# Optimization experiments

Measured on AMD Instinct MI355X. Metric: run time of the kernel, lower is better.

Reference implementation:

```python
import jax, jax.numpy as jnp
import numpy as np

GRID_SIZE = 5
GRID_RANGE = (-1.0, 1.0)


def setup_inputs() -> dict:
    key = jax.random.key(0)
    k1, k2, k3 = jax.random.split(key, 3)
    B, D, U, K = 16384, 1024, 128, GRID_SIZE + 3  # spline_order=3
    x = jax.random.normal(k1, (B, D), dtype=jnp.float32)
    # glorot-ish scale for weights
    base_weight = jax.random.normal(k2, (D, U), dtype=jnp.float32) * (1.0 / np.sqrt(D))
    spline_weight = jax.random.normal(k3, (D, U, K), dtype=jnp.float32) * (1.0 / np.sqrt(D))
    return {"x": x, "base_weight": base_weight, "spline_weight": spline_weight}


def reference(x, base_weight, spline_weight):
    # base path: SiLU(x @ W_b)
    base_out = jax.nn.silu(x @ base_weight)  # [B, U]
    # spline path: RBF over grid centers, then contract (note: x_norm in the
    # original call() is computed but unused, so it is omitted here)
    centers = jnp.linspace(GRID_RANGE[0], GRID_RANGE[1], GRID_SIZE)  # [G]
    dist = jnp.square(x[..., None] - centers)        # [B, D, G]
    rbf = jnp.exp(-5.0 * dist)                        # [B, D, G]
    spline_out = jnp.einsum('big,iug->bu', rbf, spline_weight[:, :, :GRID_SIZE])
    return base_out + spline_out
```

## Files before the change

### kernel.cpp

```cpp
#include <hip/hip_runtime.h>

typedef unsigned short u16;
typedef unsigned int u32;
typedef __bf16 bf16x8 __attribute__((ext_vector_type(8)));
typedef float f32x16 __attribute__((ext_vector_type(16)));

#define C2 (-7.213475204444817f)
#define T1C 0.28650480f
#define T2C 0.0067379470f

__device__ __forceinline__ u16 f2bf(float f) {
  u32 u = __float_as_uint(f);
  return (u16)((u + 0x7FFFu + ((u >> 16) & 1u)) >> 16);
}

__device__ __forceinline__ void async16(const void* g, void* l) {
  __builtin_amdgcn_global_load_lds(
      (const __attribute__((address_space(1))) u32*)g,
      (__attribute__((address_space(3))) u32*)l, 16, 0, 0);
}

__device__ __forceinline__ f32x16 mfma16(uint4 a, uint4 b, f32x16 c) {
  return __builtin_amdgcn_mfma_f32_32x32x16_bf16(
      __builtin_bit_cast(bf16x8, a), __builtin_bit_cast(bf16x8, b), c, 0, 0, 0);
}

__global__ __launch_bounds__(256) void kan_prep(const float* __restrict__ wb,
                                                const float* __restrict__ ws,
                                                u16* __restrict__ wst) {
  __shared__ __align__(16) u16 tile[6][32][40];
  const int t = threadIdx.x;
  const int d0 = blockIdx.x * 32;
  const int u0 = blockIdx.y * 32;
#pragma unroll
  for (int it = 0; it < 4; ++it) {
    int e = it * 256 + t;
    int uu = e & 31, dd = e >> 5;
    const float* p = ws + ((size_t)(d0 + dd) * 128 + (u0 + uu)) * 8;
    float4 v0 = *(const float4*)p;
    float g4 = p[4];
    tile[0][uu][dd] = f2bf(v0.x);
    tile[1][uu][dd] = f2bf(v0.y);
    tile[2][uu][dd] = f2bf(v0.z);
    tile[3][uu][dd] = f2bf(v0.w);
    tile[4][uu][dd] = f2bf(g4);
    tile[5][uu][dd] = f2bf(wb[(size_t)(d0 + dd) * 128 + (u0 + uu)]);
  }
  __syncthreads();
#pragma unroll
  for (int it = 0; it < 3; ++it) {
    int v = it * 256 + t;
    int s = v >> 7;
    int r = v & 127;
    int uu = r >> 2, dseg = r & 3;
    uint4 val = *(const uint4*)&tile[s][uu][dseg * 8];
    *(uint4*)(wst + (size_t)(s * 128 + u0 + uu) * 1024 + d0 + dseg * 8) = val;
  }
}

__global__ __launch_bounds__(512, 2) void kan_main(const float* __restrict__ x,
                                                   const u16* __restrict__ wst,
                                                   float* __restrict__ out) {
  __shared__ __align__(16) u16 lds[73728];
  char* ldsb = (char*)&lds[0];

  const int t = threadIdx.x;
  const int lane = t & 63;
  const int w = t >> 6;
  const int wm = w >> 2;
  const int wn = w & 3;
  const int b0 = blockIdx.x * 64;

  f32x16 accb, accs;
#pragma unroll
  for (int i = 0; i < 16; ++i) { accb[i] = 0.f; accs[i] = 0.f; }

  const int rr = t >> 3, h = t & 7;
  const int rsr = rr >> 1;
  const u32 aw_off = (u32)(rsr * 128 +
                           (((((rr & 1) << 2) | (h >> 1)) ^ (rsr & 7)) << 4) +
                           ((h & 1) << 3));
  const float* xbase = x + (size_t)(b0 + rr) * 1024 + h * 4;

  const int dR = t >> 3, dq = t & 7;
  const int dv = dq ^ (dR & 7);
  const int durow = 2 * dR + (dv >> 2);
  const int dseg = dv & 3;
  const u16* dsrc0 = wst + ((size_t)durow << 10) + dseg * 8;

  const int ml = lane & 31, kh = lane >> 5;
  const int ar = wm * 32 + ml, asr = ar >> 1;
  const u32 aoff0 = (u32)(asr * 128 + (((((ar & 1) << 2) | kh) ^ (asr & 7)) << 4));
  const u32 aoff1 = (u32)(asr * 128 + (((((ar & 1) << 2) | (2 + kh)) ^ (asr & 7)) << 4));
  const int br = wn * 32 + ml, bsr = br >> 1;
  const u32 boff0 = (u32)(24576 + bsr * 128 + (((((br & 1) << 2) | kh) ^ (bsr & 7)) << 4));
  const u32 boff1 = (u32)(24576 + bsr * 128 + (((((br & 1) << 2) | (2 + kh)) ^ (bsr & 7)) << 4));

  auto dma_weights = [&](int k0, char* buf) {
#pragma unroll
    for (int i = 0; i < 6; ++i) {
      async16(dsrc0 + ((size_t)i << 17) + k0, buf + 24576 + ((i * 512 + t) << 4));
    }
  };
  auto rbf_write = [&](char* buf, float4 xa) {
    float xf[4] = {xa.x, xa.y, xa.z, xa.w};
    float rv[6][4];
#pragma unroll
    for (int e = 0; e < 4; ++e) {
      float xv = xf[e];
      float t0 = C2 * xv;
      float P = __builtin_amdgcn_exp2f(t0 * xv);
      float Qp = __builtin_amdgcn_exp2f(-t0);
      float Qm = __builtin_amdgcn_exp2f(t0);
      float PQ = P * Qp, PQm = P * Qm;
      rv[0][e] = PQm * Qm * T2C;
      rv[1][e] = PQm * T1C;
      rv[2][e] = P;
      rv[3][e] = PQ * T1C;
      rv[4][e] = PQ * Qp * T2C;
      rv[5][e] = xv;
    }
#pragma unroll
    for (int s = 0; s < 6; ++s) {
      uint2 pk;
      pk.x = (u32)f2bf(rv[s][0]) | ((u32)f2bf(rv[s][1]) << 16);
      pk.y = (u32)f2bf(rv[s][2]) | ((u32)f2bf(rv[s][3]) << 16);
      *(uint2*)(buf + s * 4096 + aw_off) = pk;
    }
  };

  float4 xreg = *(const float4*)(xbase);
  dma_weights(0, ldsb);
  rbf_write(ldsb, xreg);
  xreg = *(const float4*)(xbase + 32);
  __syncthreads();

  for (int k = 0; k < 32; ++k) {
    char* cb = ldsb + (size_t)(k & 1) * 73728;
    if (k < 31) {
      char* nb = ldsb + (size_t)((k + 1) & 1) * 73728;
      dma_weights((k + 1) * 32, nb);
      rbf_write(nb, xreg);
    }
    if (k < 30) xreg = *(const float4*)(xbase + (k + 2) * 32);

#pragma unroll
    for (int s = 0; s < 6; ++s) {
      uint4 a0 = *(const uint4*)(cb + s * 4096 + aoff0);
      uint4 b0v = *(const uint4*)(cb + s * 8192 + boff0);
      uint4 a1 = *(const uint4*)(cb + s * 4096 + aoff1);
      uint4 b1v = *(const uint4*)(cb + s * 8192 + boff1);
      if (s < 5) {
        accs = mfma16(a0, b0v, accs);
        accs = mfma16(a1, b1v, accs);
      } else {
        accb = mfma16(a0, b0v, accb);
        accb = mfma16(a1, b1v, accb);
      }
    }
    __syncthreads();
  }

  const int n = wn * 32 + ml;
#pragma unroll
  for (int reg = 0; reg < 16; ++reg) {
    int row = (reg & 3) + 8 * (reg >> 2) + 4 * kh;
    int m = b0 + wm * 32 + row;
    float z = accb[reg];
    float sv = z / (1.0f + __expf(-z));
    out[(size_t)m * 128 + n] = sv + accs[reg];
  }
}

extern "C" void kernel_launch(void* const* d_in, const int* in_sizes, int n_in,
                              void* d_out, int out_size, void* d_ws, size_t ws_size,
                              hipStream_t stream) {
  const float* x  = (const float*)d_in[0];
  const float* wb = (const float*)d_in[1];
  const float* ws = (const float*)d_in[2];
  u16* wst = (u16*)d_ws;
  float* out = (float*)d_out;

  kan_prep<<<dim3(32, 4), 256, 0, stream>>>(wb, ws, wst);
  kan_main<<<dim3(256), 512, 0, stream>>>(x, wst, out);
}
```

Baseline: 147.1 us.

## Build RBF A-fragments in registers and split output columns across blocks

The main kernel now computes the RBF/bf16 A operands straight into MFMA fragment registers instead of staging them through LDS, so LDS holds only the double-buffered weight tiles. The 128 output columns are split across two blocks of 256 threads each, with a block-index swizzle so both halves of the same row tile run close together and share x in L2. This cuts LDS footprint and A-side LDS traffic and allows more resident blocks. In exchange each x element is loaded and its RBF features computed twice, and bf16 rounding becomes a simple round-half-up byte permute.

```diff
diff --git a/kernel.cpp b/kernel.cpp
--- a/kernel.cpp
+++ b/kernel.cpp
@@ -58,117 +58,116 @@
   }
 }
 
-__global__ __launch_bounds__(512, 2) void kan_main(const float* __restrict__ x,
+__global__ __launch_bounds__(256, 2) void kan_main(const float* __restrict__ x,
                                                    const u16* __restrict__ wst,
                                                    float* __restrict__ out) {
-  __shared__ __align__(16) u16 lds[73728];
-  char* ldsb = (char*)&lds[0];
+  __shared__ __align__(16) u16 Bs[2][6][2][2][64][8];
+  char* bsf = (char*)&Bs[0][0][0][0][0][0];
 
   const int t = threadIdx.x;
   const int lane = t & 63;
   const int w = t >> 6;
-  const int wm = w >> 2;
-  const int wn = w & 3;
-  const int b0 = blockIdx.x * 64;
+  const int wm = w >> 1, wn = w & 1;
+  const int ml = lane & 31, kh = lane >> 5;
+
+  const int bx = blockIdx.x;
+  const int mt = (bx & 7) | ((bx >> 4) << 3);
+  const int nh = (bx >> 3) & 1;
+  const int b0 = mt * 64;
+  const int u0 = nh * 64;
 
   f32x16 accb, accs;
 #pragma unroll
   for (int i = 0; i < 16; ++i) { accb[i] = 0.f; accs[i] = 0.f; }
 
-  const int rr = t >> 3, h = t & 7;
-  const int rsr = rr >> 1;
-  const u32 aw_off = (u32)(rsr * 128 +
-                           (((((rr & 1) << 2) | (h >> 1)) ^ (rsr & 7)) << 4) +
-                           ((h & 1) << 3));
-  const float* xbase = x + (size_t)(b0 + rr) * 1024 + h * 4;
+  const u16* dsrc = wst + (size_t)(u0 + ((t >> 6) & 1) * 32 + (t & 31)) * 1024 +
+                    ((t >> 7) << 4) + (((t >> 5) & 1) << 3);
 
-  const int dR = t >> 3, dq = t & 7;
-  const int dv = dq ^ (dR & 7);
-  const int durow = 2 * dR + (dv >> 2);
-  const int dseg = dv & 3;
-  const u16* dsrc0 = wst + ((size_t)durow << 10) + dseg * 8;
+  const float* xp = x + (size_t)(b0 + wm * 32 + ml) * 1024 + kh * 8;
 
-  const int ml = lane & 31, kh = lane >> 5;
-  const int ar = wm * 32 + ml, asr = ar >> 1;
-  const u32 aoff0 = (u32)(asr * 128 + (((((ar & 1) << 2) | kh) ^ (asr & 7)) << 4));
-  const u32 aoff1 = (u32)(asr * 128 + (((((ar & 1) << 2) | (2 + kh)) ^ (asr & 7)) << 4));
-  const int br = wn * 32 + ml, bsr = br >> 1;
-  const u32 boff0 = (u32)(24576 + bsr * 128 + (((((br & 1) << 2) | kh) ^ (bsr & 7)) << 4));
-  const u32 boff1 = (u32)(24576 + bsr * 128 + (((((br & 1) << 2) | (2 + kh)) ^ (bsr & 7)) << 4));
+  auto dma = [&](int k0, int buf) {
+    const u16* s0 = dsrc + k0;
+    char* d0 = bsf + buf * 24576 + t * 16;
+#pragma unroll
+    for (int s = 0; s < 6; ++s) async16(s0 + (size_t)s * 131072, d0 + s * 4096);
+  };
 
-  auto dma_weights = [&](int k0, char* buf) {
+  auto mkfrags = [&](float4 a, float4 b, uint4* fr) {
+    float xf[8] = {a.x, a.y, a.z, a.w, b.x, b.y, b.z, b.w};
+    u32 rb[6][8];
 #pragma unroll
-    for (int i = 0; i < 6; ++i) {
-      async16(dsrc0 + ((size_t)i << 17) + k0, buf + 24576 + ((i * 512 + t) << 4));
-    }
-  };
-  auto rbf_write = [&](char* buf, float4 xa) {
-    float xf[4] = {xa.x, xa.y, xa.z, xa.w};
-    float rv[6][4];
-#pragma unroll
-    for (int e = 0; e < 4; ++e) {
+    for (int e = 0; e < 8; ++e) {
       float xv = xf[e];
       float t0 = C2 * xv;
       float P = __builtin_amdgcn_exp2f(t0 * xv);
       float Qp = __builtin_amdgcn_exp2f(-t0);
       float Qm = __builtin_amdgcn_exp2f(t0);
       float PQ = P * Qp, PQm = P * Qm;
-      rv[0][e] = PQm * Qm * T2C;
-      rv[1][e] = PQm * T1C;
-      rv[2][e] = P;
-      rv[3][e] = PQ * T1C;
-      rv[4][e] = PQ * Qp * T2C;
-      rv[5][e] = xv;
+      rb[0][e] = __float_as_uint(PQm * Qm * T2C) + 0x8000u;
+      rb[1][e] = __float_as_uint(PQm * T1C) + 0x8000u;
+      rb[2][e] = __float_as_uint(P) + 0x8000u;
+      rb[3][e] = __float_as_uint(PQ * T1C) + 0x8000u;
+      rb[4][e] = __float_as_uint(PQ * Qp * T2C) + 0x8000u;
+      rb[5][e] = __float_as_uint(xv) + 0x8000u;
     }
 #pragma unroll
     for (int s = 0; s < 6; ++s) {
-      uint2 pk;
-      pk.x = (u32)f2bf(rv[s][0]) | ((u32)f2bf(rv[s][1]) << 16);
-      pk.y = (u32)f2bf(rv[s][2]) | ((u32)f2bf(rv[s][3]) << 16);
-      *(uint2*)(buf + s * 4096 + aw_off) = pk;
+      fr[s].x = __builtin_amdgcn_perm(rb[s][1], rb[s][0], 0x07060302);
+      fr[s].y = __builtin_amdgcn_perm(rb[s][3], rb[s][2], 0x07060302);
+      fr[s].z = __builtin_amdgcn_perm(rb[s][5], rb[s][4], 0x07060302);
+      fr[s].w = __builtin_amdgcn_perm(rb[s][7], rb[s][6], 0x07060302);
     }
   };
 
-  float4 xreg = *(const float4*)(xbase);
-  dma_weights(0, ldsb);
-  rbf_write(ldsb, xreg);
-  xreg = *(const float4*)(xbase + 32);
+  float4 xc0 = *(const float4*)(xp + 0);
+  float4 xc1 = *(const float4*)(xp + 4);
+  float4 xc2 = *(const float4*)(xp + 16);
+  float4 xc3 = *(const float4*)(xp + 20);
+  dma(0, 0);
   __syncthreads();
 
+  u32 bufoff = 0;
   for (int k = 0; k < 32; ++k) {
-    char* cb = ldsb + (size_t)(k & 1) * 73728;
+    float4 xn0, xn1, xn2, xn3;
     if (k < 31) {
-      char* nb = ldsb + (size_t)((k + 1) & 1) * 73728;
-      dma_weights((k + 1) * 32, nb);
-      rbf_write(nb, xreg);
+      dma((k + 1) * 32, (k + 1) & 1);
+      const float* xq = xp + (k + 1) * 32;
+      xn0 = *(const float4*)(xq + 0);
+      xn1 = *(const float4*)(xq + 4);
+      xn2 = *(const float4*)(xq + 16);
+      xn3 = *(const float4*)(xq + 20);
     }
-    if (k < 30) xreg = *(const float4*)(xbase + (k + 2) * 32);
 
+    uint4 fr0[6], fr1[6];
+    mkfrags(xc0, xc1, fr0);
+    mkfrags(xc2, xc3, fr1);
+
+    const char* bb = bsf + bufoff + wn * 1024 + lane * 16;
 #pragma unroll
     for (int s = 0; s < 6; ++s) {
-      uint4 a0 = *(const uint4*)(cb + s * 4096 + aoff0);
-      uint4 b0v = *(const uint4*)(cb + s * 8192 + boff0);
-      uint4 a1 = *(const uint4*)(cb + s * 4096 + aoff1);
-      uint4 b1v = *(const uint4*)(cb + s * 8192 + boff1);
+      uint4 b0v = *(const uint4*)(bb + s * 4096);
+      uint4 b1v = *(const uint4*)(bb + s * 4096 + 2048);
       if (s < 5) {
-        accs = mfma16(a0, b0v, accs);
-        accs = mfma16(a1, b1v, accs);
+        accs = mfma16(fr0[s], b0v, accs);
+        accs = mfma16(fr1[s], b1v, accs);
       } else {
-        accb = mfma16(a0, b0v, accb);
-        accb = mfma16(a1, b1v, accb);
+        accb = mfma16(fr0[s], b0v, accb);
+        accb = mfma16(fr1[s], b1v, accb);
       }
     }
     __syncthreads();
+    bufoff ^= 24576;
+    xc0 = xn0; xc1 = xn1; xc2 = xn2; xc3 = xn3;
   }
 
-  const int n = wn * 32 + ml;
+  const int nq = u0 + wn * 32 + ml;
 #pragma unroll
   for (int reg = 0; reg < 16; ++reg) {
     int row = (reg & 3) + 8 * (reg >> 2) + 4 * kh;
     int m = b0 + wm * 32 + row;
     float z = accb[reg];
     float sv = z / (1.0f + __expf(-z));
-    out[(size_t)m * 128 + n] = sv + accs[reg];
+    out[(size_t)m * 128 + nq] = sv + accs[reg];
   }
 }
 
@@ -182,5 +181,5 @@
   float* out = (float*)d_out;
 
   kan_prep<<<dim3(32, 4), 256, 0, stream>>>(wb, ws, wst);
-  kan_main<<<dim3(256), 512, 0, stream>>>(x, wst, out);
+  kan_main<<<dim3(512), 256, 0, stream>>>(x, wst, out);
 }
```

Measured after the change: 173.2 us. 17.7% more time.
